# Performance work log

Measured on AMD Instinct MI355X. Metric: run time of the kernel, lower is better.

Reference implementation:

```python
import jax, jax.numpy as jnp
import numpy as np
import math

CHANNELS = 512
OUT_CHANNELS = 512
N_HEADS = 8
WINDOW = 4
K_CH = CHANNELS // N_HEADS


def _conv1x1(x, W, b):
    # x: (B, C_in, T), W: (C_out, C_in), b: (C_out,)
    return jnp.einsum('oc,bct->bot', W, x) + b[None, :, None]


def _get_relative_embeddings(emb, length, window=WINDOW):
    # emb: (H, 2*window+1, k_ch) -> (H, 2*length-1, k_ch)
    pad_length = max(length - (window + 1), 0)
    start = max(window + 1 - length, 0)
    e = jnp.pad(emb, ((0, 0), (pad_length, pad_length), (0, 0))) if pad_length > 0 else emb
    return e[:, start:start + 2 * length - 1]


def _relative_to_absolute(x):
    # x: (B, H, L, 2L-1) -> (B, H, L, L)
    b, h, L, _ = x.shape
    x = jnp.pad(x, ((0, 0), (0, 0), (0, 0), (0, 1)))          # (B,H,L,2L)
    xf = x.reshape(b, h, L * 2 * L)
    xf = jnp.pad(xf, ((0, 0), (0, 0), (L - 1, 0)))
    return xf.reshape(b, h, L + 1, 2 * L - 1)[:, :, :L, L - 1:]


def _absolute_to_relative(x):
    # x: (B, H, L, L) -> (B, H, L, 2L-1)
    b, h, L, _ = x.shape
    x = jnp.pad(x, ((0, 0), (0, 0), (0, 0), (0, L - 1)))       # (B,H,L,2L-1)
    xf = x.reshape(b, h, L * (2 * L - 1))
    xf = jnp.pad(xf, ((0, 0), (0, 0), (L, 0)))
    return xf.reshape(b, h, L, 2 * L)[:, :, :, 1:]


def setup_inputs() -> dict:
    key = jax.random.key(0)
    ks = jax.random.split(key, 16)
    B, C, T = 4, CHANNELS, 1024
    xavier = math.sqrt(2.0 / (C + C))
    rel_std = K_CH ** -0.5
    return {
        'x_q': jax.random.normal(ks[0], (B, C, T), jnp.float32),
        'x_k': jax.random.normal(ks[1], (B, C, T), jnp.float32),
        'x_v': jax.random.normal(ks[2], (B, C, T), jnp.float32),
        'Wq': jax.random.normal(ks[3], (C, C), jnp.float32) * xavier,
        'bq': jnp.zeros((C,), jnp.float32),
        'Wk': jax.random.normal(ks[4], (C, C), jnp.float32) * xavier,
        'bk': jnp.zeros((C,), jnp.float32),
        'Wv': jax.random.normal(ks[5], (C, C), jnp.float32) * xavier,
        'bv': jnp.zeros((C,), jnp.float32),
        'Wo': jax.random.normal(ks[6], (OUT_CHANNELS, C), jnp.float32) * xavier,
        'bo': jnp.zeros((OUT_CHANNELS,), jnp.float32),
        'emb_rel_k': jax.random.normal(ks[7], (N_HEADS, 2 * WINDOW + 1, K_CH), jnp.float32) * rel_std,
        'emb_rel_v': jax.random.normal(ks[8], (N_HEADS, 2 * WINDOW + 1, K_CH), jnp.float32) * rel_std,
    }


def reference(x_q, x_k, x_v, Wq, bq, Wk, bk, Wv, bv, Wo, bo, emb_rel_k, emb_rel_v):
    q = _conv1x1(x_q, Wq, bq)
    k = _conv1x1(x_k, Wk, bk)
    v = _conv1x1(x_v, Wv, bv)
    B, C, T = q.shape
    # (B, C, T) -> (B, H, T, k_ch); head h owns contiguous k_ch channel chunk
    qh = q.reshape(B, N_HEADS, K_CH, T).transpose(0, 1, 3, 2) / math.sqrt(K_CH)
    kh = k.reshape(B, N_HEADS, K_CH, T).transpose(0, 1, 3, 2)
    vh = v.reshape(B, N_HEADS, K_CH, T).transpose(0, 1, 3, 2)
    scores = jnp.einsum('bhtd,bhsd->bhts', qh, kh)              # (B,H,T,T)
    rel_k = _get_relative_embeddings(emb_rel_k, T)              # (H,2T-1,d)
    rel_logits = jnp.einsum('bhtd,hmd->bhtm', qh, rel_k)        # (B,H,T,2T-1)
    scores = scores + _relative_to_absolute(rel_logits)
    attn = jax.nn.softmax(scores, axis=-1)
    ctx = jnp.einsum('bhts,bhsd->bhtd', attn, vh)
    rel_w = _absolute_to_relative(attn)                         # (B,H,T,2T-1)
    rel_v = _get_relative_embeddings(emb_rel_v, T)
    ctx = ctx + jnp.einsum('bhtm,hmd->bhtd', rel_w, rel_v)
    out = ctx.transpose(0, 1, 3, 2).reshape(B, C, T)
    return _conv1x1(out, Wo, bo)
```

## Files before the change

### kernel.cpp

```cpp
#include <hip/hip_runtime.h>

#define T_LEN 1024
#define NH 8
#define DH 64
#define CCH 512
#define LOG2E 1.44269504088896340736f

typedef _Float16 f16;
typedef _Float16 f16x8 __attribute__((ext_vector_type(8)));
typedef _Float16 f16x4 __attribute__((ext_vector_type(4)));
typedef float f32x4 __attribute__((ext_vector_type(4)));

__device__ __forceinline__ void dma16(const void* g, void* l)
{
    __builtin_amdgcn_global_load_lds((const __attribute__((address_space(1))) void*)g,
                                     (__attribute__((address_space(3))) void*)l, 16, 0, 0);
}

__global__ __launch_bounds__(256)
void prep_kernel(const float* __restrict__ x0, const float* __restrict__ x1,
                 const float* __restrict__ x2, const float* __restrict__ W0,
                 const float* __restrict__ W1, const float* __restrict__ W2,
                 const float* __restrict__ W3, f16* __restrict__ o0,
                 f16* __restrict__ o1, f16* __restrict__ o2, f16* __restrict__ w0,
                 f16* __restrict__ w1, f16* __restrict__ w2, f16* __restrict__ w3,
                 int B)
{
    const int z = blockIdx.z;
    if (z < 3 * B) {
        const int t0 = blockIdx.x * 64, c0 = blockIdx.y * 64;
        const int which = z / B, b = z % B;
        const float* x = (which == 0) ? x0 : (which == 1) ? x1 : x2;
        f16* o = (which == 0) ? o0 : (which == 1) ? o1 : o2;

        __shared__ float L[64 * 68];
        const int cl = threadIdx.x & 63, g = threadIdx.x >> 6;
        const float* src = x + ((size_t)(b * CCH + c0 + cl)) * T_LEN + t0 + g * 16;
        #pragma unroll
        for (int j = 0; j < 4; ++j)
            *(float4*)&L[cl * 68 + g * 16 + 4 * j] = *(const float4*)&src[4 * j];
        __syncthreads();
        const int tl = threadIdx.x & 63, cg = (threadIdx.x >> 6) * 16;
        f16 h[16];
        #pragma unroll
        for (int j = 0; j < 16; ++j) h[j] = (f16)L[(cg + j) * 68 + tl];
        f16* dst = o + ((size_t)(b * T_LEN + t0 + tl)) * CCH + c0 + cg;
        *(f16x8*)&dst[0] = *(f16x8*)&h[0];
        *(f16x8*)&dst[8] = *(f16x8*)&h[8];
    } else {
        const int slice = z - 3 * B;
        size_t i = ((size_t)(slice * 128 + blockIdx.y * 16 + blockIdx.x) * 256 + threadIdx.x) * 4;
        const int wi = (int)(i >> 18);
        const size_t off = i & 262143;
        const float* src = (wi == 0) ? W0 : (wi == 1) ? W1 : (wi == 2) ? W2 : W3;
        f16* dst = (wi == 0) ? w0 : (wi == 1) ? w1 : (wi == 2) ? w2 : w3;
        float4 v4 = *(const float4*)&src[off];
        f16x4 h = {(f16)v4.x, (f16)v4.y, (f16)v4.z, (f16)v4.w};
        *(f16x4*)&dst[off] = h;
    }
}

__global__ __launch_bounds__(256)
void proj_qkv(const f16* __restrict__ xq, const f16* __restrict__ xk,
              const f16* __restrict__ xv, const f16* __restrict__ wq,
              const f16* __restrict__ wk, const f16* __restrict__ wv,
              const float* __restrict__ bq, const float* __restrict__ bk,
              const float* __restrict__ bv, f16* __restrict__ qo,
              f16* __restrict__ ko, f16* __restrict__ vo)
{
    const int which = blockIdx.z;
    const f16* X = (which == 0) ? xq : (which == 1) ? xk : xv;
    const f16* W = (which == 0) ? wq : (which == 1) ? wk : wv;
    const float* bias = (which == 0) ? bq : (which == 1) ? bk : bv;
    const float scale = (which == 0) ? 0.125f * LOG2E : 1.0f;

    const int r0 = blockIdx.x * 128;
    const int o0 = blockIdx.y * 128;
    const int tid = threadIdx.x;
    const int w = tid >> 6, lane = tid & 63;
    const int quad = lane >> 4, l15 = lane & 15;
    const int a  = w >> 1;
    const int b2 = w & 1;

    __shared__ __align__(16) f16 Xs[128 * 64];
    __shared__ __align__(16) f16 Wsh[128 * 64];

    const int srow = tid >> 3;
    const int scol = ((tid & 7) ^ (srow & 7)) << 3;

    const f16* Xg = X + (size_t)(r0 + srow) * CCH + scol;
    const f16* Wg = W + (size_t)(o0 + srow) * CCH + scol;

    const int ax = (which < 2) ? a : b2;
    const int aw = (which < 2) ? b2 : a;

    f32x4 acc[4][4] = {};

    for (int kc = 0; kc < 8; ++kc) {
        if (kc) __syncthreads();
        const int c1 = kc * 64;
        #pragma unroll
        for (int jj = 0; jj < 4; ++jj) {
            dma16(Xg + c1 + (size_t)(32 * jj) * CCH, &Xs[((size_t)tid + 256 * jj) * 8]);
            dma16(Wg + c1 + (size_t)(32 * jj) * CCH, &Wsh[((size_t)tid + 256 * jj) * 8]);
        }
        __syncthreads();

        #pragma unroll
        for (int ks = 0; ks < 2; ++ks) {
            const int sl = ((ks * 4 + quad) ^ (l15 & 7)) << 3;
            f16x8 xf[4], wf[4];
            #pragma unroll
            for (int i = 0; i < 4; ++i)
                xf[i] = *(const f16x8*)&Xs[(64 * ax + 16 * i + l15) * 64 + sl];
            #pragma unroll
            for (int j = 0; j < 4; ++j)
                wf[j] = *(const f16x8*)&Wsh[(64 * aw + 16 * j + l15) * 64 + sl];
            if (which < 2) {
                #pragma unroll
                for (int i = 0; i < 4; ++i)
                    #pragma unroll
                    for (int j = 0; j < 4; ++j)
                        acc[i][j] = __builtin_amdgcn_mfma_f32_16x16x32_f16(
                            xf[i], wf[j], acc[i][j], 0, 0, 0);
            } else {
                #pragma unroll
                for (int i = 0; i < 4; ++i)
                    #pragma unroll
                    for (int j = 0; j < 4; ++j)
                        acc[i][j] = __builtin_amdgcn_mfma_f32_16x16x32_f16(
                            wf[i], xf[j], acc[i][j], 0, 0, 0);
            }
        }
    }

    if (which < 2) {
        f16* out = (which == 0) ? qo : ko;
        float bl[4];
        #pragma unroll
        for (int j = 0; j < 4; ++j) bl[j] = bias[o0 + 64 * b2 + 16 * j + l15];
        #pragma unroll
        for (int i = 0; i < 4; ++i)
            #pragma unroll
            for (int r = 0; r < 4; ++r) {
                size_t row = (size_t)(r0 + 64 * a + 16 * i + 4 * quad + r) * CCH;
                #pragma unroll
                for (int j = 0; j < 4; ++j)
                    out[row + o0 + 64 * b2 + 16 * j + l15] =
                        (f16)((acc[i][j][r] + bl[j]) * scale);
            }
    } else {
        const int bb = r0 >> 10, tb = r0 & 1023;
        #pragma unroll
        for (int i = 0; i < 4; ++i) {
            float4 bv4 = *(const float4*)&bias[o0 + 64 * a + 16 * i + 4 * quad];
            float bl[4] = {bv4.x, bv4.y, bv4.z, bv4.w};
            #pragma unroll
            for (int r = 0; r < 4; ++r) {
                size_t row = ((size_t)(bb * CCH + o0 + 64 * a + 16 * i + 4 * quad + r)) * T_LEN;
                #pragma unroll
                for (int j = 0; j < 4; ++j)
                    vo[row + tb + 64 * b2 + 16 * j + l15] =
                        (f16)(acc[i][j][r] + bl[r]);
            }
        }
    }
}

__global__ __launch_bounds__(256)
void attn_mfma(const f16* __restrict__ q, const f16* __restrict__ kk,
               const f16* __restrict__ v, const float* __restrict__ ekg,
               const float* __restrict__ evg, f16* __restrict__ ctx)
{
    const int t0 = blockIdx.x * 64, h = blockIdx.y, b = blockIdx.z;
    const int tid = threadIdx.x;
    const int w = tid >> 6, lane = tid & 63;
    const int quad = lane >> 4, l15 = lane & 15;

    __shared__ __align__(16) f16 Qs[4096], Ps[4096];
    __shared__ __align__(16) f16 Ks[2][4096], Vs[2][4096];
    __shared__ float eks[576], evs[576];
    __shared__ float ls[64];

    const int srow = tid >> 3;
    const int scol = ((tid & 7) ^ (srow & 7)) << 3;

    for (int i = tid; i < 576; i += 256) {
        eks[i] = ekg[h * 576 + i];
        evs[i] = evg[h * 576 + i];
    }

    const f16* gk = kk + ((size_t)(b * T_LEN + srow)) * CCH + h * DH + scol;
    const f16* gv = v + ((size_t)(b * CCH + h * DH + srow)) * T_LEN + scol;

    dma16(q + ((size_t)(b * T_LEN + t0 + srow)) * CCH + h * DH + scol, &Qs[(size_t)tid * 8]);
    dma16(q + ((size_t)(b * T_LEN + t0 + srow + 32)) * CCH + h * DH + scol, &Qs[((size_t)tid + 256) * 8]);
    dma16(gk, &Ks[0][(size_t)tid * 8]);
    dma16(gk + (size_t)32 * CCH, &Ks[0][((size_t)tid + 256) * 8]);
    dma16(gv, &Vs[0][(size_t)tid * 8]);
    dma16(gv + (size_t)32 * T_LEN, &Vs[0][((size_t)tid + 256) * 8]);
    __syncthreads();

    f16x8 qf[2];
    #pragma unroll
    for (int ks = 0; ks < 2; ++ks)
        qf[ks] = *(const f16x8*)&Qs[(16 * w + l15) * 64 + (((ks * 4 + quad) ^ (l15 & 7)) << 3)];

    const int myt = 16 * w + l15;
    float Ssum = 0.f;
    f32x4 O[4] = {};

    const bool corner_hi = (blockIdx.x == 0);
    const bool corner_lo = (blockIdx.x == 15);

    for (int it = 0; it < 16; ++it) {
        const int kb = it, cb = it & 1;
        if (it) __syncthreads();

        if (it < 15) {
            const int nb = cb ^ 1;
            dma16(gk + (size_t)((it + 1) * 64) * CCH, &Ks[nb][(size_t)tid * 8]);
            dma16(gk + (size_t)((it + 1) * 64 + 32) * CCH, &Ks[nb][((size_t)tid + 256) * 8]);
            dma16(gv + (it + 1) * 64, &Vs[nb][(size_t)tid * 8]);
            dma16(gv + (size_t)32 * T_LEN + (it + 1) * 64, &Vs[nb][((size_t)tid + 256) * 8]);
        }

        f32x4 S[4] = {};
        #pragma unroll
        for (int ks = 0; ks < 2; ++ks) {
            #pragma unroll
            for (int ct = 0; ct < 4; ++ct) {
                f16x8 aa = *(const f16x8*)&Ks[cb][(16 * ct + l15) * 64 + (((ks * 4 + quad) ^ (l15 & 7)) << 3)];
                S[ct] = __builtin_amdgcn_mfma_f32_16x16x32_f16(aa, qf[ks], S[ct], 0, 0, 0);
            }
        }

        if ((corner_hi && kb == 15) || (corner_lo && kb == 0)) {
            const int s0g = kb * 64;
            #pragma unroll
            for (int ct = 0; ct < 4; ++ct)
                #pragma unroll
                for (int r = 0; r < 4; ++r) {
                    int t_g = t0 + myt;
                    int s_g = s0g + 16 * ct + 4 * quad + r;
                    int df = s_g - t_g;
                    if (df >= 1019 && df <= 1023) {
                        const float* ekp = &eks[(df - 1019) * 64];
                        float sacc = 0.f;
                        for (int d = 0; d < 64; ++d)
                            sacc += (float)Qs[myt * 64 + (((d >> 3) ^ (myt & 7)) << 3) + (d & 7)] * ekp[d];
                        S[ct][r] += sacc;
                    } else if (df >= -1023 && df <= -1021) {
                        const float* ekp = &eks[(1029 + df) * 64];
                        const int t2 = myt - 1;
                        float sacc = 0.f;
                        for (int d = 0; d < 64; ++d)
                            sacc += (float)Qs[t2 * 64 + (((d >> 3) ^ (t2 & 7)) << 3) + (d & 7)] * ekp[d];
                        S[ct][r] += sacc;
                    }
                }
        }

        #pragma unroll
        for (int ct = 0; ct < 4; ++ct) {
            f16x4 pk_;
            #pragma unroll
            for (int r = 0; r < 4; ++r) {
                float p = exp2f(S[ct][r]);
                Ssum += p;
                pk_[r] = (f16)p;
            }
            int colh = (((2 * ct + (quad >> 1)) ^ (myt & 7)) << 3) + (quad & 1) * 4;
            *(f16x4*)&Ps[myt * 64 + colh] = pk_;
        }

        #pragma unroll
        for (int ks = 0; ks < 2; ++ks) {
            f16x8 aa = *(const f16x8*)&Ps[(16 * w + l15) * 64 + (((ks * 4 + quad) ^ (l15 & 7)) << 3)];
            #pragma unroll
            for (int ct = 0; ct < 4; ++ct) {
                f16x8 bf = *(const f16x8*)&Vs[cb][(16 * ct + l15) * 64 + (((ks * 4 + quad) ^ (l15 & 7)) << 3)];
                O[ct] = __builtin_amdgcn_mfma_f32_16x16x32_f16(aa, bf, O[ct], 0, 0, 0);
            }
        }

        const int s0g = kb * 64;
        if (s0g <= t0 + 67 && s0g + 63 >= t0 - 4) {
            #pragma unroll
            for (int r = 0; r < 4; ++r) {
                int t_loc = 16 * w + 4 * quad + r;
                int t_g = t0 + t_loc;
                int slo = max(s0g, t_g - 4), shi = min(s0g + 63, t_g + 4);
                for (int s = slo; s <= shi; ++s) {
                    int sl = s - s0g;
                    float p = (float)Ps[t_loc * 64 + (((sl >> 3) ^ (t_loc & 7)) << 3) + (sl & 7)];
                    const float* evp = &evs[(s - t_g + 4) * 64];
                    #pragma unroll
                    for (int ct = 0; ct < 4; ++ct)
                        O[ct][r] += p * evp[16 * ct + l15];
                }
            }
        }
    }

    Ssum += __shfl_xor(Ssum, 16);
    Ssum += __shfl_xor(Ssum, 32);
    if (quad == 0) ls[myt] = 1.0f / Ssum;
    __syncthreads();

    #pragma unroll
    for (int r = 0; r < 4; ++r) {
        const int t_loc = 16 * w + 4 * quad + r;
        const float rl = ls[t_loc];
        size_t rowo = ((size_t)(b * T_LEN + t0 + t_loc)) * CCH + h * DH;
        #pragma unroll
        for (int ct = 0; ct < 4; ++ct)
            ctx[rowo + 16 * ct + l15] = (f16)(O[ct][r] * rl);
    }
}

__global__ __launch_bounds__(256)
void proj_out(const f16* __restrict__ ctx, const f16* __restrict__ Wo,
              const float* __restrict__ bo, float* __restrict__ out)
{
    const int r0 = blockIdx.x * 128;
    const int o0 = blockIdx.y * 128;
    const int tid = threadIdx.x;
    const int w = tid >> 6, lane = tid & 63;
    const int quad = lane >> 4, l15 = lane & 15;
    const int a  = w >> 1;
    const int b2 = w & 1;

    __shared__ __align__(16) f16 Cs[128 * 64];
    __shared__ __align__(16) f16 Wsh[128 * 64];

    const int srow = tid >> 3;
    const int scol = ((tid & 7) ^ (srow & 7)) << 3;

    const f16* Cg = ctx + (size_t)(r0 + srow) * CCH + scol;
    const f16* Wg = Wo + (size_t)(o0 + srow) * CCH + scol;

    f32x4 acc[4][4] = {};

    for (int kc = 0; kc < 8; ++kc) {
        if (kc) __syncthreads();
        const int c1 = kc * 64;
        #pragma unroll
        for (int jj = 0; jj < 4; ++jj) {
            dma16(Cg + c1 + (size_t)(32 * jj) * CCH, &Cs[((size_t)tid + 256 * jj) * 8]);
            dma16(Wg + c1 + (size_t)(32 * jj) * CCH, &Wsh[((size_t)tid + 256 * jj) * 8]);
        }
        __syncthreads();

        #pragma unroll
        for (int ks = 0; ks < 2; ++ks) {
            const int sl = ((ks * 4 + quad) ^ (l15 & 7)) << 3;
            f16x8 wf[4], cf[4];
            #pragma unroll
            for (int i = 0; i < 4; ++i)
                wf[i] = *(const f16x8*)&Wsh[(64 * a + 16 * i + l15) * 64 + sl];
            #pragma unroll
            for (int j = 0; j < 4; ++j)
                cf[j] = *(const f16x8*)&Cs[(64 * b2 + 16 * j + l15) * 64 + sl];
            #pragma unroll
            for (int i = 0; i < 4; ++i)
                #pragma unroll
                for (int j = 0; j < 4; ++j)
                    acc[i][j] = __builtin_amdgcn_mfma_f32_16x16x32_f16(
                        wf[i], cf[j], acc[i][j], 0, 0, 0);
        }
    }

    const int bb = r0 >> 10, tb = r0 & 1023;
    #pragma unroll
    for (int i = 0; i < 4; ++i) {
        float4 bv4 = *(const float4*)&bo[o0 + 64 * a + 16 * i + 4 * quad];
        float bl[4] = {bv4.x, bv4.y, bv4.z, bv4.w};
        #pragma unroll
        for (int r = 0; r < 4; ++r) {
            size_t row = ((size_t)(bb * CCH + o0 + 64 * a + 16 * i + 4 * quad + r)) * T_LEN;
            #pragma unroll
            for (int j = 0; j < 4; ++j)
                out[row + tb + 64 * b2 + 16 * j + l15] = acc[i][j][r] + bl[r];
        }
    }
}

extern "C" void kernel_launch(void* const* d_in, const int* in_sizes, int n_in,
                              void* d_out, int out_size, void* d_ws, size_t ws_size,
                              hipStream_t stream)
{
    const float* x_q = (const float*)d_in[0];
    const float* x_k = (const float*)d_in[1];
    const float* x_v = (const float*)d_in[2];
    const float* Wq  = (const float*)d_in[3];
    const float* bq  = (const float*)d_in[4];
    const float* Wk  = (const float*)d_in[5];
    const float* bk  = (const float*)d_in[6];
    const float* Wv  = (const float*)d_in[7];
    const float* bv  = (const float*)d_in[8];
    const float* Wo  = (const float*)d_in[9];
    const float* bo  = (const float*)d_in[10];
    const float* erk = (const float*)d_in[11];
    const float* erv = (const float*)d_in[12];

    const int B = in_sizes[0] / (CCH * T_LEN);
    const size_t te = (size_t)B * CCH * T_LEN;
    const size_t we = (size_t)CCH * CCH;

    f16* p = (f16*)d_ws;
    f16* xTq = p; p += te;
    f16* xTk = p; p += te;
    f16* xTv = p; p += te;
    f16* wqh = p; p += we;
    f16* wkh = p; p += we;
    f16* wvh = p; p += we;
    f16* woh = p; p += we;
    f16* qh  = p; p += te;
    f16* kh  = p; p += te;
    f16* vh  = p; p += te;
    f16* ch  = p; p += te;

    dim3 blk(256);
    prep_kernel<<<dim3(16, 8, 3 * B + 8), blk, 0, stream>>>(
        x_q, x_k, x_v, Wq, Wk, Wv, Wo, xTq, xTk, xTv, wqh, wkh, wvh, woh, B);
    proj_qkv<<<dim3(B * 8, 4, 3), blk, 0, stream>>>(
        xTq, xTk, xTv, wqh, wkh, wvh, bq, bk, bv, qh, kh, vh);
    attn_mfma<<<dim3(T_LEN / 64, NH, B), blk, 0, stream>>>(
        qh, kh, vh, erk, erv, ch);
    proj_out<<<dim3(B * 8, 4), blk, 0, stream>>>(
        ch, woh, bo, (float*)d_out);
}
```

Before: 152.2 us.

## Double attention query tile to 128 rows and halve proj_out row tile

Result: slower. 178.0 us (+17.0%).

```diff
diff --git a/kernel.cpp b/kernel.cpp
--- a/kernel.cpp
+++ b/kernel.cpp
@@ -172,15 +172,15 @@
                const f16* __restrict__ v, const float* __restrict__ ekg,
                const float* __restrict__ evg, f16* __restrict__ ctx)
 {
-    const int t0 = blockIdx.x * 64, h = blockIdx.y, b = blockIdx.z;
+    const int t0 = blockIdx.x * 128, h = blockIdx.y, b = blockIdx.z;
     const int tid = threadIdx.x;
     const int w = tid >> 6, lane = tid & 63;
     const int quad = lane >> 4, l15 = lane & 15;
 
-    __shared__ __align__(16) f16 Qs[4096], Ps[4096];
+    __shared__ __align__(16) f16 Qs[8192], Ps[8192];
     __shared__ __align__(16) f16 Ks[2][4096], Vs[2][4096];
     __shared__ float eks[576], evs[576];
-    __shared__ float ls[64];
+    __shared__ float ls[128];
 
     const int srow = tid >> 3;
     const int scol = ((tid & 7) ^ (srow & 7)) << 3;
@@ -193,25 +193,31 @@
     const f16* gk = kk + ((size_t)(b * T_LEN + srow)) * CCH + h * DH + scol;
     const f16* gv = v + ((size_t)(b * CCH + h * DH + srow)) * T_LEN + scol;
 
-    dma16(q + ((size_t)(b * T_LEN + t0 + srow)) * CCH + h * DH + scol, &Qs[(size_t)tid * 8]);
-    dma16(q + ((size_t)(b * T_LEN + t0 + srow + 32)) * CCH + h * DH + scol, &Qs[((size_t)tid + 256) * 8]);
+    #pragma unroll
+    for (int jj = 0; jj < 4; ++jj)
+        dma16(q + ((size_t)(b * T_LEN + t0 + srow + 32 * jj)) * CCH + h * DH + scol,
+              &Qs[((size_t)tid + 256 * jj) * 8]);
     dma16(gk, &Ks[0][(size_t)tid * 8]);
     dma16(gk + (size_t)32 * CCH, &Ks[0][((size_t)tid + 256) * 8]);
     dma16(gv, &Vs[0][(size_t)tid * 8]);
     dma16(gv + (size_t)32 * T_LEN, &Vs[0][((size_t)tid + 256) * 8]);
     __syncthreads();
 
-    f16x8 qf[2];
+    const int row0 = 32 * w;
+    f16x8 qf[2][2];
     #pragma unroll
-    for (int ks = 0; ks < 2; ++ks)
-        qf[ks] = *(const f16x8*)&Qs[(16 * w + l15) * 64 + (((ks * 4 + quad) ^ (l15 & 7)) << 3)];
-
-    const int myt = 16 * w + l15;
-    float Ssum = 0.f;
-    f32x4 O[4] = {};
+    for (int m = 0; m < 2; ++m)
+        #pragma unroll
+        for (int ks = 0; ks < 2; ++ks)
+            qf[m][ks] = *(const f16x8*)&Qs[(row0 + 16 * m + l15) * 64 +
+                                           (((ks * 4 + quad) ^ (l15 & 7)) << 3)];
+
+    const int myt = row0 + l15;
+    float Ssum[2] = {0.f, 0.f};
+    f32x4 O[2][4] = {};
 
     const bool corner_hi = (blockIdx.x == 0);
-    const bool corner_lo = (blockIdx.x == 15);
+    const bool corner_lo = (blockIdx.x == 7);
 
     for (int it = 0; it < 16; ++it) {
         const int kb = it, cb = it & 1;
@@ -225,105 +231,132 @@
             dma16(gv + (size_t)32 * T_LEN + (it + 1) * 64, &Vs[nb][((size_t)tid + 256) * 8]);
         }
 
-        f32x4 S[4] = {};
+        f32x4 S[2][4] = {};
         #pragma unroll
         for (int ks = 0; ks < 2; ++ks) {
             #pragma unroll
             for (int ct = 0; ct < 4; ++ct) {
-                f16x8 aa = *(const f16x8*)&Ks[cb][(16 * ct + l15) * 64 + (((ks * 4 + quad) ^ (l15 & 7)) << 3)];
-                S[ct] = __builtin_amdgcn_mfma_f32_16x16x32_f16(aa, qf[ks], S[ct], 0, 0, 0);
+                f16x8 aa = *(const f16x8*)&Ks[cb][(16 * ct + l15) * 64 +
+                                                  (((ks * 4 + quad) ^ (l15 & 7)) << 3)];
+                #pragma unroll
+                for (int m = 0; m < 2; ++m)
+                    S[m][ct] = __builtin_amdgcn_mfma_f32_16x16x32_f16(
+                        aa, qf[m][ks], S[m][ct], 0, 0, 0);
             }
         }
 
         if ((corner_hi && kb == 15) || (corner_lo && kb == 0)) {
             const int s0g = kb * 64;
             #pragma unroll
-            for (int ct = 0; ct < 4; ++ct)
+            for (int m = 0; m < 2; ++m) {
+                const int tq = myt + 16 * m;
+                #pragma unroll
+                for (int ct = 0; ct < 4; ++ct)
+                    #pragma unroll
+                    for (int r = 0; r < 4; ++r) {
+                        int t_g = t0 + tq;
+                        int s_g = s0g + 16 * ct + 4 * quad + r;
+                        int df = s_g - t_g;
+                        if (df >= 1019 && df <= 1023) {
+                            const float* ekp = &eks[(df - 1019) * 64];
+                            float sacc = 0.f;
+                            for (int d = 0; d < 64; ++d)
+                                sacc += (float)Qs[tq * 64 + (((d >> 3) ^ (tq & 7)) << 3) + (d & 7)] * ekp[d];
+                            S[m][ct][r] += sacc;
+                        } else if (df >= -1023 && df <= -1021) {
+                            const float* ekp = &eks[(1029 + df) * 64];
+                            const int t2 = tq - 1;
+                            float sacc = 0.f;
+                            for (int d = 0; d < 64; ++d)
+                                sacc += (float)Qs[t2 * 64 + (((d >> 3) ^ (t2 & 7)) << 3) + (d & 7)] * ekp[d];
+                            S[m][ct][r] += sacc;
+                        }
+                    }
+            }
+        }
+
+        #pragma unroll
+        for (int m = 0; m < 2; ++m) {
+            const int tq = myt + 16 * m;
+            #pragma unroll
+            for (int ct = 0; ct < 4; ++ct) {
+                f16x4 pk_;
                 #pragma unroll
                 for (int r = 0; r < 4; ++r) {
-                    int t_g = t0 + myt;
-                    int s_g = s0g + 16 * ct + 4 * quad + r;
-                    int df = s_g - t_g;
-                    if (df >= 1019 && df <= 1023) {
-                        const float* ekp = &eks[(df - 1019) * 64];
-                        float sacc = 0.f;
-                        for (int d = 0; d < 64; ++d)
-                            sacc += (float)Qs[myt * 64 + (((d >> 3) ^ (myt & 7)) << 3) + (d & 7)] * ekp[d];
-                        S[ct][r] += sacc;
-                    } else if (df >= -1023 && df <= -1021) {
-                        const float* ekp = &eks[(1029 + df) * 64];
-                        const int t2 = myt - 1;
-                        float sacc = 0.f;
-                        for (int d = 0; d < 64; ++d)
-                            sacc += (float)Qs[t2 * 64 + (((d >> 3) ^ (t2 & 7)) << 3) + (d & 7)] * ekp[d];
-                        S[ct][r] += sacc;
+                    float p = exp2f(S[m][ct][r]);
+                    Ssum[m] += p;
+                    pk_[r] = (f16)p;
+                }
+                int colh = (((2 * ct + (quad >> 1)) ^ (tq & 7)) << 3) + (quad & 1) * 4;
+                *(f16x4*)&Ps[tq * 64 + colh] = pk_;
+            }
+        }
+
+        #pragma unroll
+        for (int ks = 0; ks < 2; ++ks) {
+            f16x8 aa[2];
+            #pragma unroll
+            for (int m = 0; m < 2; ++m)
+                aa[m] = *(const f16x8*)&Ps[(row0 + 16 * m + l15) * 64 +
+                                           (((ks * 4 + quad) ^ (l15 & 7)) << 3)];
+            #pragma unroll
+            for (int ct = 0; ct < 4; ++ct) {
+                f16x8 bf = *(const f16x8*)&Vs[cb][(16 * ct + l15) * 64 +
+                                                  (((ks * 4 + quad) ^ (l15 & 7)) << 3)];
+                #pragma unroll
+                for (int m = 0; m < 2; ++m)
+                    O[m][ct] = __builtin_amdgcn_mfma_f32_16x16x32_f16(
+                        aa[m], bf, O[m][ct], 0, 0, 0);
+            }
+        }
+
+        const int s0g = kb * 64;
+        if (s0g <= t0 + 131 && s0g + 63 >= t0 - 4) {
+            #pragma unroll
+            for (int m = 0; m < 2; ++m)
+                #pragma unroll
+                for (int r = 0; r < 4; ++r) {
+                    int t_loc = row0 + 16 * m + 4 * quad + r;
+                    int t_g = t0 + t_loc;
+                    int slo = max(s0g, t_g - 4), shi = min(s0g + 63, t_g + 4);
+                    for (int s = slo; s <= shi; ++s) {
+                        int sl = s - s0g;
+                        float p = (float)Ps[t_loc * 64 + (((sl >> 3) ^ (t_loc & 7)) << 3) + (sl & 7)];
+                        const float* evp = &evs[(s - t_g + 4) * 64];
+                        #pragma unroll
+                        for (int ct = 0; ct < 4; ++ct)
+                            O[m][ct][r] += p * evp[16 * ct + l15];
                     }
                 }
         }
-
-        #pragma unroll
-        for (int ct = 0; ct < 4; ++ct) {
-            f16x4 pk_;
-            #pragma unroll
-            for (int r = 0; r < 4; ++r) {
-                float p = exp2f(S[ct][r]);
-                Ssum += p;
-                pk_[r] = (f16)p;
-            }
-            int colh = (((2 * ct + (quad >> 1)) ^ (myt & 7)) << 3) + (quad & 1) * 4;
-            *(f16x4*)&Ps[myt * 64 + colh] = pk_;
-        }
-
-        #pragma unroll
-        for (int ks = 0; ks < 2; ++ks) {
-            f16x8 aa = *(const f16x8*)&Ps[(16 * w + l15) * 64 + (((ks * 4 + quad) ^ (l15 & 7)) << 3)];
-            #pragma unroll
-            for (int ct = 0; ct < 4; ++ct) {
-                f16x8 bf = *(const f16x8*)&Vs[cb][(16 * ct + l15) * 64 + (((ks * 4 + quad) ^ (l15 & 7)) << 3)];
-                O[ct] = __builtin_amdgcn_mfma_f32_16x16x32_f16(aa, bf, O[ct], 0, 0, 0);
-            }
-        }
-
-        const int s0g = kb * 64;
-        if (s0g <= t0 + 67 && s0g + 63 >= t0 - 4) {
-            #pragma unroll
-            for (int r = 0; r < 4; ++r) {
-                int t_loc = 16 * w + 4 * quad + r;
-                int t_g = t0 + t_loc;
-                int slo = max(s0g, t_g - 4), shi = min(s0g + 63, t_g + 4);
-                for (int s = slo; s <= shi; ++s) {
-                    int sl = s - s0g;
-                    float p = (float)Ps[t_loc * 64 + (((sl >> 3) ^ (t_loc & 7)) << 3) + (sl & 7)];
-                    const float* evp = &evs[(s - t_g + 4) * 64];
-                    #pragma unroll
-                    for (int ct = 0; ct < 4; ++ct)
-                        O[ct][r] += p * evp[16 * ct + l15];
-                }
-            }
-        }
-    }
-
-    Ssum += __shfl_xor(Ssum, 16);
-    Ssum += __shfl_xor(Ssum, 32);
-    if (quad == 0) ls[myt] = 1.0f / Ssum;
+    }
+
+    #pragma unroll
+    for (int m = 0; m < 2; ++m) {
+        Ssum[m] += __shfl_xor(Ssum[m], 16);
+        Ssum[m] += __shfl_xor(Ssum[m], 32);
+        if (quad == 0) ls[row0 + 16 * m + l15] = 1.0f / Ssum[m];
+    }
     __syncthreads();
 
     #pragma unroll
-    for (int r = 0; r < 4; ++r) {
-        const int t_loc = 16 * w + 4 * quad + r;
-        const float rl = ls[t_loc];
-        size_t rowo = ((size_t)(b * T_LEN + t0 + t_loc)) * CCH + h * DH;
-        #pragma unroll
-        for (int ct = 0; ct < 4; ++ct)
-            ctx[rowo + 16 * ct + l15] = (f16)(O[ct][r] * rl);
-    }
+    for (int m = 0; m < 2; ++m)
+        #pragma unroll
+        for (int r = 0; r < 4; ++r) {
+            const int t_loc = row0 + 16 * m + 4 * quad + r;
+            const float rl = ls[t_loc];
+            size_t rowo = ((size_t)(b * T_LEN + t0 + t_loc)) * CCH + h * DH;
+            #pragma unroll
+            for (int ct = 0; ct < 4; ++ct)
+                ctx[rowo + 16 * ct + l15] = (f16)(O[m][ct][r] * rl);
+        }
 }
 
 __global__ __launch_bounds__(256)
 void proj_out(const f16* __restrict__ ctx, const f16* __restrict__ Wo,
               const float* __restrict__ bo, float* __restrict__ out)
 {
-    const int r0 = blockIdx.x * 128;
+    const int r0 = blockIdx.x * 64;
     const int o0 = blockIdx.y * 128;
     const int tid = threadIdx.x;
     const int w = tid >> 6, lane = tid & 63;
@@ -331,7 +364,7 @@
     const int a  = w >> 1;
     const int b2 = w & 1;
 
-    __shared__ __align__(16) f16 Cs[128 * 64];
+    __shared__ __align__(16) f16 Cs[64 * 64];
     __shared__ __align__(16) f16 Wsh[128 * 64];
 
     const int srow = tid >> 3;
@@ -340,32 +373,33 @@
     const f16* Cg = ctx + (size_t)(r0 + srow) * CCH + scol;
     const f16* Wg = Wo + (size_t)(o0 + srow) * CCH + scol;
 
-    f32x4 acc[4][4] = {};
+    f32x4 acc[4][2] = {};
 
     for (int kc = 0; kc < 8; ++kc) {
         if (kc) __syncthreads();
         const int c1 = kc * 64;
         #pragma unroll
-        for (int jj = 0; jj < 4; ++jj) {
+        for (int jj = 0; jj < 4; ++jj)
+            dma16(Wg + c1 + (size_t)(32 * jj) * CCH, &Wsh[((size_t)tid + 256 * jj) * 8]);
+        #pragma unroll
+        for (int jj = 0; jj < 2; ++jj)
             dma16(Cg + c1 + (size_t)(32 * jj) * CCH, &Cs[((size_t)tid + 256 * jj) * 8]);
-            dma16(Wg + c1 + (size_t)(32 * jj) * CCH, &Wsh[((size_t)tid + 256 * jj) * 8]);
-        }
         __syncthreads();
 
         #pragma unroll
         for (int ks = 0; ks < 2; ++ks) {
             const int sl = ((ks * 4 + quad) ^ (l15 & 7)) << 3;
-            f16x8 wf[4], cf[4];
+            f16x8 wf[4], cf[2];
             #pragma unroll
             for (int i = 0; i < 4; ++i)
                 wf[i] = *(const f16x8*)&Wsh[(64 * a + 16 * i + l15) * 64 + sl];
             #pragma unroll
-            for (int j = 0; j < 4; ++j)
-                cf[j] = *(const f16x8*)&Cs[(64 * b2 + 16 * j + l15) * 64 + sl];
+            for (int j = 0; j < 2; ++j)
+                cf[j] = *(const f16x8*)&Cs[(32 * b2 + 16 * j + l15) * 64 + sl];
             #pragma unroll
             for (int i = 0; i < 4; ++i)
                 #pragma unroll
-                for (int j = 0; j < 4; ++j)
+                for (int j = 0; j < 2; ++j)
                     acc[i][j] = __builtin_amdgcn_mfma_f32_16x16x32_f16(
                         wf[i], cf[j], acc[i][j], 0, 0, 0);
         }
@@ -380,8 +414,8 @@
         for (int r = 0; r < 4; ++r) {
             size_t row = ((size_t)(bb * CCH + o0 + 64 * a + 16 * i + 4 * quad + r)) * T_LEN;
             #pragma unroll
-            for (int j = 0; j < 4; ++j)
-                out[row + tb + 64 * b2 + 16 * j + l15] = acc[i][j][r] + bl[r];
+            for (int j = 0; j < 2; ++j)
+                out[row + tb + 32 * b2 + 16 * j + l15] = acc[i][j][r] + bl[r];
         }
     }
 }
@@ -426,8 +460,8 @@
         x_q, x_k, x_v, Wq, Wk, Wv, Wo, xTq, xTk, xTv, wqh, wkh, wvh, woh, B);
     proj_qkv<<<dim3(B * 8, 4, 3), blk, 0, stream>>>(
         xTq, xTk, xTv, wqh, wkh, wvh, bq, bk, bv, qh, kh, vh);
-    attn_mfma<<<dim3(T_LEN / 64, NH, B), blk, 0, stream>>>(
+    attn_mfma<<<dim3(T_LEN / 128, NH, B), blk, 0, stream>>>(
         qh, kh, vh, erk, erv, ch);
-    proj_out<<<dim3(B * 8, 4), blk, 0, stream>>>(
+    proj_out<<<dim3(B * 16, 4), blk, 0, stream>>>(
         ch, woh, bo, (float*)d_out);
 }
```
